# Kernel optimization log

Hardware: AMD Instinct MI355X
Metric: run time of the kernel (lower is better)

The kernel has to match this reference:

```python
import jax, jax.numpy as jnp
import numpy as np


def setup_inputs() -> dict:
    key = jax.random.key(0)
    k1, k2, k3, k4 = jax.random.split(key, 4)
    B, S, D = 4, 2048, 1024
    scale = 1.0 / np.sqrt(D)
    x = jax.random.normal(k1, (B, S, D), dtype=jnp.float32)
    Wq = jax.random.normal(k2, (D, D), dtype=jnp.float32) * scale
    Wk = jax.random.normal(k3, (D, D), dtype=jnp.float32) * scale
    Wv = jax.random.normal(k4, (D, D), dtype=jnp.float32) * scale
    return {"x": x, "Wq": Wq, "Wk": Wk, "Wv": Wv}


def reference(x, Wq, Wk, Wv):
    # x: [B, S, D]; Wq/Wk/Wv: [d_out, d_in] torch Linear convention (y = x @ W.T)
    B, S, D = x.shape
    q = jnp.einsum('bsd,od->bso', x, Wq)
    k = jnp.einsum('bsd,od->bso', x, Wk)
    v = jnp.einsum('bsd,od->bso', x, Wv)
    scores = jnp.einsum('bqo,bko->bqk', q, k)  # [B, S, S]
    causal = jnp.tril(jnp.ones((S, S), dtype=bool))  # True = keep
    scores = jnp.where(causal, scores, -jnp.inf)
    d_out = q.shape[-1]
    attn = jax.nn.softmax(scores / jnp.sqrt(jnp.asarray(d_out, x.dtype)), axis=-1)
    # dropout_prob = 0.0 -> identity
    return jnp.einsum('bqk,bko->bqo', attn, v)
```

## Files before the change

### kernel.cpp

```cpp
#include <hip/hip_runtime.h>
#include <hip/hip_bf16.h>
#include <stdint.h>

typedef __attribute__((ext_vector_type(8))) short bf16x8;
typedef __attribute__((ext_vector_type(4))) float f32x4;

__device__ __forceinline__ float bf2f(unsigned short u) {
    union { unsigned int i; float f; } z; z.i = ((unsigned int)u) << 16; return z.f;
}
__device__ __forceinline__ unsigned short f2bf(float f) {
    union { float f; unsigned int i; } z; z.f = f;
    unsigned int x = z.i;
    unsigned int r = x + 0x7fffu + ((x >> 16) & 1u);
    return (unsigned short)(r >> 16);
}

typedef const __attribute__((address_space(1))) unsigned int* gp_t;
typedef __attribute__((address_space(3))) unsigned int* lp_t;

__device__ __forceinline__ void gload_lds16(const void* g, void* l) {
    __builtin_amdgcn_global_load_lds((gp_t)g, (lp_t)l, 16, 0, 0);
}

__device__ __forceinline__ int xcd_remap(int orig, int nwg) {
    const int q = nwg >> 3, r = nwg & 7;
    const int xcd = orig & 7, pos = orig >> 3;
    return (xcd < r ? xcd * (q + 1) : r * (q + 1) + (xcd - r) * q) + pos;
}

__global__ __launch_bounds__(256) void cvt_all(
    const float* __restrict__ x, const float* __restrict__ wq,
    const float* __restrict__ wk, const float* __restrict__ wv,
    unsigned short* __restrict__ xb, unsigned short* __restrict__ wqkv) {
    const int NX = 1 << 21;
    const int DD4 = 1 << 18;
    const int total = NX + 3 * DD4;
    int i = blockIdx.x * 256 + threadIdx.x;
    const int stride = gridDim.x * 256;
    for (; i < total; i += stride) {
        const float* src;
        ushort4* dst;
        float scale = 1.0f;
        int idx;
        if (i < NX) {
            src = x; dst = (ushort4*)xb; idx = i;
        } else {
            const int j = i - NX;
            const int r = j >> 18;
            src = (r == 0) ? wq : (r == 1) ? wk : wv;
            if (r == 0) scale = 0.03125f;
            dst = (ushort4*)wqkv + (size_t)r * DD4;
            idx = j & (DD4 - 1);
            dst -= (size_t)0;
            dst += 0;
        }
        float4 v = reinterpret_cast<const float4*>(src)[idx];
        ushort4 u;
        u.x = f2bf(v.x * scale); u.y = f2bf(v.y * scale);
        u.z = f2bf(v.z * scale); u.w = f2bf(v.w * scale);
        dst[idx] = u;
    }
}

#define MFMA(a, b, c) __builtin_amdgcn_mfma_f32_16x16x32_bf16(a, b, c, 0, 0, 0)
#define SB() __builtin_amdgcn_sched_barrier(0)
#define BAR() __builtin_amdgcn_s_barrier()
#define LGKM0() asm volatile("s_waitcnt lgkmcnt(0)" ::: "memory")

__device__ __forceinline__ void gemm256_core(
    const unsigned short* __restrict__ Ab,
    const unsigned short* __restrict__ Bb,
    int m0, int n0,
    unsigned short (&As)[2][256 * 64], unsigned short (&Bs)[2][256 * 64],
    f32x4 (&acc)[8][4])
{
    constexpr int LD = 1024, NK = 16;
    const int tid = threadIdx.x;
    const int l = tid & 63, w = tid >> 6;
    const int wr = w >> 2, wc = w & 3;

    const int srow = w * 8 + (l >> 3);
    const int scol = ((l & 7) ^ (l >> 3)) * 8;
    const size_t ldst = (size_t)w * 1024 + (size_t)l * 16;

    auto stageA = [&](int t, int h, int b) {
        const unsigned short* src = Ab + (size_t)(m0 + h * 128 + srow) * LD + t * 64 + scol;
        char* dst = (char*)&As[b][0] + h * 16384 + ldst;
        gload_lds16(src, dst);
        gload_lds16(src + (size_t)64 * LD, dst + 8192);
    };
    auto stageB = [&](int t, int h, int b) {
        const unsigned short* src = Bb + (size_t)(n0 + h * 128 + srow) * LD + t * 64 + scol;
        char* dst = (char*)&Bs[b][0] + h * 16384 + ldst;
        gload_lds16(src, dst);
        gload_lds16(src + (size_t)64 * LD, dst + 8192);
    };

    const int l15 = l & 15, l7 = l & 7;
    const int s0 = (((l >> 4) ^ l7) * 16);
    const int s1 = ((((l >> 4) + 4) ^ l7) * 16);

    bf16x8 Af[4][2], Bf0[2][2], Bf1[2][2];

    stageA(0, 0, 0); stageA(0, 1, 0); stageB(0, 0, 0); stageB(0, 1, 0);
    stageB(1, 0, 1); stageB(1, 1, 1);
    asm volatile("s_waitcnt vmcnt(4)" ::: "memory");
    SB(); BAR(); SB();

    for (int t = 0; t < NK; ++t) {
        const int b = t & 1, bn = b ^ 1;
        const char* ab = (const char*)&As[b][0] + (wr * 128 + l15) * 128;
        const char* bb = (const char*)&Bs[b][0] + (wc * 64 + l15) * 128;

        #pragma unroll
        for (int mi = 0; mi < 4; ++mi) {
            Af[mi][0] = *(const bf16x8*)(ab + mi * 2048 + s0);
            Af[mi][1] = *(const bf16x8*)(ab + mi * 2048 + s1);
        }
        #pragma unroll
        for (int ni = 0; ni < 2; ++ni) {
            Bf0[ni][0] = *(const bf16x8*)(bb + ni * 2048 + s0);
            Bf0[ni][1] = *(const bf16x8*)(bb + ni * 2048 + s1);
        }
        if (t + 1 < NK) stageA(t + 1, 0, bn);
        BAR(); LGKM0(); SB();
        __builtin_amdgcn_s_setprio(1);
        #pragma unroll
        for (int mi = 0; mi < 4; ++mi)
            #pragma unroll
            for (int ni = 0; ni < 2; ++ni) {
                acc[mi][ni] = MFMA(Af[mi][0], Bf0[ni][0], acc[mi][ni]);
                acc[mi][ni] = MFMA(Af[mi][1], Bf0[ni][1], acc[mi][ni]);
            }
        __builtin_amdgcn_s_setprio(0);
        SB(); BAR(); SB();

        #pragma unroll
        for (int ni = 0; ni < 2; ++ni) {
            Bf1[ni][0] = *(const bf16x8*)(bb + 4096 + ni * 2048 + s0);
            Bf1[ni][1] = *(const bf16x8*)(bb + 4096 + ni * 2048 + s1);
        }
        if (t + 1 < NK) stageA(t + 1, 1, bn);
        BAR(); LGKM0(); SB();
        __builtin_amdgcn_s_setprio(1);
        #pragma unroll
        for (int mi = 0; mi < 4; ++mi)
            #pragma unroll
            for (int ni = 0; ni < 2; ++ni) {
                acc[mi][2 + ni] = MFMA(Af[mi][0], Bf1[ni][0], acc[mi][2 + ni]);
                acc[mi][2 + ni] = MFMA(Af[mi][1], Bf1[ni][1], acc[mi][2 + ni]);
            }
        __builtin_amdgcn_s_setprio(0);
        SB(); BAR(); SB();

        #pragma unroll
        for (int mi = 0; mi < 4; ++mi) {
            Af[mi][0] = *(const bf16x8*)(ab + 8192 + mi * 2048 + s0);
            Af[mi][1] = *(const bf16x8*)(ab + 8192 + mi * 2048 + s1);
        }
        if (t + 2 < NK) stageB(t + 2, 0, b);
        BAR(); LGKM0(); SB();
        __builtin_amdgcn_s_setprio(1);
        #pragma unroll
        for (int mi = 0; mi < 4; ++mi)
            #pragma unroll
            for (int ni = 0; ni < 2; ++ni) {
                acc[4 + mi][2 + ni] = MFMA(Af[mi][0], Bf1[ni][0], acc[4 + mi][2 + ni]);
                acc[4 + mi][2 + ni] = MFMA(Af[mi][1], Bf1[ni][1], acc[4 + mi][2 + ni]);
            }
        __builtin_amdgcn_s_setprio(0);
        SB(); BAR(); SB();

        if (t + 2 < NK) stageB(t + 2, 1, b);
        BAR(); SB();
        __builtin_amdgcn_s_setprio(1);
        #pragma unroll
        for (int mi = 0; mi < 4; ++mi)
            #pragma unroll
            for (int ni = 0; ni < 2; ++ni) {
                acc[4 + mi][ni] = MFMA(Af[mi][0], Bf0[ni][0], acc[4 + mi][ni]);
                acc[4 + mi][ni] = MFMA(Af[mi][1], Bf0[ni][1], acc[4 + mi][ni]);
            }
        __builtin_amdgcn_s_setprio(0);
        if (t + 2 < NK) {
            asm volatile("s_waitcnt vmcnt(4)" ::: "memory");
        } else if (t + 1 < NK) {
            asm volatile("s_waitcnt vmcnt(0)" ::: "memory");
        }
        SB(); BAR(); SB();
    }
}

__global__ __launch_bounds__(512, 2) void qk_proj(
    const unsigned short* __restrict__ xb, const unsigned short* __restrict__ wqkv,
    unsigned short* __restrict__ qb, unsigned short* __restrict__ kb)
{
    const int wg = xcd_remap(blockIdx.x, 256);
    const int mt = wg & 31, nt = wg >> 5;
    const int m0 = mt * 256, n0 = nt * 256;

    __shared__ unsigned short As[2][256 * 64];
    __shared__ unsigned short Bs[2][256 * 64];
    f32x4 acc[8][4] = {};

    gemm256_core(xb, wqkv, m0, n0, As, Bs, acc);

    const int tid = threadIdx.x;
    const int l = tid & 63, w = tid >> 6;
    const int wr = w >> 2, wc = w & 3;
    const int crow = (l >> 4) * 4, ccol = l & 15;
    unsigned short* C = (nt < 4) ? qb : kb;
    const int cb = (nt < 4) ? n0 : n0 - 1024;
    #pragma unroll
    for (int mi = 0; mi < 8; ++mi)
        #pragma unroll
        for (int ni = 0; ni < 4; ++ni) {
            const size_t rbase = (size_t)(m0 + wr * 128 + mi * 16 + crow);
            const size_t cg = (size_t)(cb + wc * 64 + ni * 16 + ccol);
            #pragma unroll
            for (int r = 0; r < 4; ++r)
                C[(rbase + r) * 1024 + cg] = f2bf(acc[mi][ni][r]);
        }
}

__device__ __forceinline__ void gemm128_core64(
    const unsigned short* __restrict__ Ab, int lda,
    const unsigned short* __restrict__ Bb, int ldb,
    int m0, int n0, int nk,
    unsigned short (&As)[2][128 * 64], unsigned short (&Bs)[2][128 * 64],
    f32x4 (&acc)[4][4])
{
    const int tid = threadIdx.x;
    const int l = tid & 63, w = tid >> 6;
    const int wr = w >> 1, wc = w & 1;
    const int l15 = l & 15;

    const int srow = w * 8 + (l >> 3);
    const int scol = ((l & 7) ^ (l >> 3)) * 8;
    const size_t ldst = (size_t)w * 1024 + (size_t)l * 16;

    auto stage = [&](int t, int b) {
        const int k0 = t * 64;
        #pragma unroll
        for (int i = 0; i < 4; ++i) {
            gload_lds16(Ab + (size_t)(m0 + i * 32 + srow) * lda + k0 + scol,
                        (char*)&As[b][0] + i * 4096 + ldst);
            gload_lds16(Bb + (size_t)(n0 + i * 32 + srow) * ldb + k0 + scol,
                        (char*)&Bs[b][0] + i * 4096 + ldst);
        }
    };

    const int s0 = (((l >> 4) ^ (l & 7)) * 16);
    const int s1 = ((((l >> 4) + 4) ^ (l & 7)) * 16);

    stage(0, 0);
    if (nk > 1) {
        stage(1, 1);
        asm volatile("s_waitcnt vmcnt(8)" ::: "memory");
    } else {
        asm volatile("s_waitcnt vmcnt(0)" ::: "memory");
    }
    SB(); BAR(); SB();

    for (int t = 0; t < nk; ++t) {
        const int b = t & 1;
        const char* ab = (const char*)&As[b][0] + (wr * 64 + l15) * 128;
        const char* bb = (const char*)&Bs[b][0] + (wc * 64 + l15) * 128;
        bf16x8 af[4][2], bfr[4][2];
        #pragma unroll
        for (int m = 0; m < 4; ++m) {
            af[m][0] = *(const bf16x8*)(ab + m * 2048 + s0);
            af[m][1] = *(const bf16x8*)(ab + m * 2048 + s1);
        }
        #pragma unroll
        for (int n = 0; n < 4; ++n) {
            bfr[n][0] = *(const bf16x8*)(bb + n * 2048 + s0);
            bfr[n][1] = *(const bf16x8*)(bb + n * 2048 + s1);
        }
        LGKM0(); SB();
        BAR(); SB();
        if (t + 2 < nk) stage(t + 2, b);

        __builtin_amdgcn_s_setprio(1);
        #pragma unroll
        for (int m = 0; m < 4; ++m)
            #pragma unroll
            for (int n = 0; n < 4; ++n) {
                acc[m][n] = MFMA(af[m][0], bfr[n][0], acc[m][n]);
                acc[m][n] = MFMA(af[m][1], bfr[n][1], acc[m][n]);
            }
        __builtin_amdgcn_s_setprio(0);

        if (t + 2 < nk) {
            asm volatile("s_waitcnt vmcnt(8)" ::: "memory");
        } else if (t + 1 < nk) {
            asm volatile("s_waitcnt vmcnt(0)" ::: "memory");
        }
        SB(); BAR(); SB();
    }
}

__global__ __launch_bounds__(256) void v_scores128(
    const unsigned short* __restrict__ xb, const unsigned short* __restrict__ wv,
    const unsigned short* __restrict__ qb, const unsigned short* __restrict__ kb,
    unsigned short* __restrict__ vt, unsigned short* __restrict__ sc)
{
    const int wg = xcd_remap(blockIdx.x, 1056);

    __shared__ unsigned short As[2][128 * 64];
    __shared__ unsigned short Bs[2][128 * 64];
    f32x4 acc[4][4] = {};

    const int tid = threadIdx.x;
    const int l = tid & 63, w = tid >> 6;
    const int wr = w >> 1, wc = w & 1;
    const int crow = (l >> 4) * 4, ccol = l & 15;

    if (wg < 512) {
        const int mt = wg & 63, nt = wg >> 6;
        const int m0 = mt * 128, n0 = nt * 128;
        gemm128_core64(xb, 1024, wv, 1024, m0, n0, 16, As, Bs, acc);
        #pragma unroll
        for (int m = 0; m < 4; ++m)
            #pragma unroll
            for (int n = 0; n < 4; ++n) {
                const int rbase = m0 + wr * 64 + m * 16 + crow;
                const int o = n0 + wc * 64 + n * 16 + ccol;
                ushort4 u;
                u.x = f2bf(acc[m][n][0]);
                u.y = f2bf(acc[m][n][1]);
                u.z = f2bf(acc[m][n][2]);
                u.w = f2bf(acc[m][n][3]);
                *reinterpret_cast<ushort4*>(&vt[(size_t)o * 8192 + rbase]) = u;
            }
    } else {
        const int s = wg - 512;
        const int z = s / 136, r = s % 136;
        int mt = (int)((__builtin_sqrtf(8.f * r + 1.f) - 1.f) * 0.5f);
        while ((mt + 1) * (mt + 2) / 2 <= r) ++mt;
        while (mt * (mt + 1) / 2 > r) --mt;
        const int nt = r - mt * (mt + 1) / 2;
        const int m0 = mt * 128, n0 = nt * 128;
        const unsigned short* Ab = qb + (size_t)z * 2048 * 1024;
        const unsigned short* Bb = kb + (size_t)z * 2048 * 1024;
        gemm128_core64(Ab, 1024, Bb, 1024, m0, n0, 16, As, Bs, acc);
        unsigned short* C = sc + (size_t)z * 2048 * 2048;
        #pragma unroll
        for (int m = 0; m < 4; ++m)
            #pragma unroll
            for (int n = 0; n < 4; ++n) {
                const size_t rbase = (size_t)(m0 + wr * 64 + m * 16 + crow);
                const size_t cg = (size_t)(n0 + wc * 64 + n * 16 + ccol);
                #pragma unroll
                for (int r2 = 0; r2 < 4; ++r2)
                    C[(rbase + r2) * 2048 + cg] = f2bf(acc[m][n][r2]);
            }
    }
}

__global__ __launch_bounds__(256) void gemm128_pv(
    const unsigned short* __restrict__ A, int lda, long long sA,
    const unsigned short* __restrict__ B, int ldb, long long sB,
    float* __restrict__ C, int ldc, long long sC, int K)
{
    const int orig = blockIdx.x;
    const int h = orig >> 8;
    const int c = xcd_remap(orig & 255, 256);
    const int z = c >> 6;
    const int rem = c & 63;
    const int nt = rem >> 3;
    const int j = rem & 7;
    const int mt = h ? (15 - j) : j;

    const unsigned short* Ab = A + (size_t)z * sA;
    const unsigned short* Bb = B + (size_t)z * sB;
    const int Keff = ((mt + 1) * 128 < K) ? (mt + 1) * 128 : K;
    const int nk = Keff >> 6;

    __shared__ unsigned short As[2][128 * 64];
    __shared__ unsigned short Bs[2][128 * 64];
    f32x4 acc[4][4] = {};

    gemm128_core64(Ab, lda, Bb, ldb, mt * 128, nt * 128, nk, As, Bs, acc);

    const int tid = threadIdx.x;
    const int l = tid & 63, w = tid >> 6;
    const int wr = w >> 1, wc = w & 1;
    const int crow = (l >> 4) * 4, ccol = l & 15;
    float* Cb = C + (size_t)z * sC;
    #pragma unroll
    for (int m = 0; m < 4; ++m)
        #pragma unroll
        for (int n = 0; n < 4; ++n) {
            const size_t rbase = (size_t)(mt * 128 + wr * 64 + m * 16 + crow);
            const size_t cg = (size_t)(nt * 128 + wc * 64 + n * 16 + ccol);
            #pragma unroll
            for (int r = 0; r < 4; ++r)
                Cb[(rbase + r) * ldc + cg] = acc[m][n][r];
        }
}

__global__ __launch_bounds__(256) void softmax_causal(unsigned short* __restrict__ P) {
    const int S = 2048;
    const int w = threadIdx.x >> 6, l = threadIdx.x & 63;
    const int gq = blockIdx.x * 4 + w;
    const int q = gq & (S - 1);
    unsigned short* row = P + (size_t)gq * S;
    const int wlim = ((q >> 7) + 1) << 7;
    const float NEG = -__builtin_huge_valf();

    float f[4][8];
    #pragma unroll
    for (int p = 0; p < 4; ++p) {
        const int c0 = p * 512 + l * 8;
        if (p * 512 <= q && c0 <= q) {
            uint4 rv = *reinterpret_cast<const uint4*>(row + c0);
            unsigned short us[8];
            us[0] = rv.x & 0xffff; us[1] = rv.x >> 16;
            us[2] = rv.y & 0xffff; us[3] = rv.y >> 16;
            us[4] = rv.z & 0xffff; us[5] = rv.z >> 16;
            us[6] = rv.w & 0xffff; us[7] = rv.w >> 16;
            #pragma unroll
            for (int i = 0; i < 8; ++i)
                f[p][i] = (c0 + i <= q) ? bf2f(us[i]) : NEG;
        } else {
            #pragma unroll
            for (int i = 0; i < 8; ++i) f[p][i] = NEG;
        }
    }

    float m = NEG;
    #pragma unroll
    for (int p = 0; p < 4; ++p)
        #pragma unroll
        for (int i = 0; i < 8; ++i) m = fmaxf(m, f[p][i]);
    #pragma unroll
    for (int o = 1; o < 64; o <<= 1) m = fmaxf(m, __shfl_xor(m, o));

    float s = 0.f;
    #pragma unroll
    for (int p = 0; p < 4; ++p)
        #pragma unroll
        for (int i = 0; i < 8; ++i) {
            f[p][i] = exp2f((f[p][i] - m) * 1.44269504f);
            s += f[p][i];
        }
    #pragma unroll
    for (int o = 1; o < 64; o <<= 1) s += __shfl_xor(s, o);
    const float inv = 1.0f / s;

    #pragma unroll
    for (int p = 0; p < 4; ++p) {
        const int c0 = p * 512 + l * 8;
        if (p * 512 < wlim && c0 < wlim) {
            uint4 ov;
            ov.x = f2bf(f[p][0] * inv) | ((unsigned int)f2bf(f[p][1] * inv) << 16);
            ov.y = f2bf(f[p][2] * inv) | ((unsigned int)f2bf(f[p][3] * inv) << 16);
            ov.z = f2bf(f[p][4] * inv) | ((unsigned int)f2bf(f[p][5] * inv) << 16);
            ov.w = f2bf(f[p][6] * inv) | ((unsigned int)f2bf(f[p][7] * inv) << 16);
            *reinterpret_cast<uint4*>(row + c0) = ov;
        }
    }
}

extern "C" void kernel_launch(void* const* d_in, const int* in_sizes, int n_in,
                              void* d_out, int out_size, void* d_ws, size_t ws_size,
                              hipStream_t stream) {
    const float* x  = (const float*)d_in[0];
    const float* Wq = (const float*)d_in[1];
    const float* Wk = (const float*)d_in[2];
    const float* Wv = (const float*)d_in[3];
    float* out = (float*)d_out;

    const int Bz = 4, S = 2048, D = 1024;
    const int MS = Bz * S;
    const int DD = D * D;

    char* ws = (char*)d_ws;
    unsigned short* xb   = (unsigned short*)(ws);
    unsigned short* wqkv = (unsigned short*)(ws + (16ull << 20));
    unsigned short* qb   = (unsigned short*)(ws + (22ull << 20));
    unsigned short* kb   = (unsigned short*)(ws + (38ull << 20));
    unsigned short* vt   = (unsigned short*)(ws + (54ull << 20));
    unsigned short* sc   = (unsigned short*)(ws + (70ull << 20));

    cvt_all<<<2048, 256, 0, stream>>>(x, Wq, Wk, Wv, xb, wqkv);

    qk_proj<<<256, 512, 0, stream>>>(xb, wqkv, qb, kb);

    v_scores128<<<1056, 256, 0, stream>>>(xb, wqkv + (size_t)2 * DD, qb, kb, vt, sc);

    softmax_causal<<<2048, 256, 0, stream>>>(sc);

    gemm128_pv<<<512, 256, 0, stream>>>(
        sc, S, (long long)S * S, vt, MS, S, out, D, (long long)S * D, S);
}
```

Baseline: 156.8 us.

## Fold Wq and Wk into a single weight product to skip the K projection

Uses the identity q·kᵀ = x·(Wqᵀ·Wk)·xᵀ. A small 1024x1024 GEMM first forms the combined weight Wqᵀ·Wk (with the 1/32 scale folded in), and the scores are then computed as (x·W)·xᵀ. This removes one of the two D×D projections over the 8192 tokens and drops the separate Q and K buffers. The V projection moves into the same launch as T=x·W, at the cost of a transpose kernel, an extra tiny GEMM, and an extra bf16 rounding of the product weight.

```diff
diff --git a/kernel.cpp b/kernel.cpp
--- a/kernel.cpp
+++ b/kernel.cpp
@@ -28,37 +28,61 @@
     return (xcd < r ? xcd * (q + 1) : r * (q + 1) + (xcd - r) * q) + pos;
 }
 
-__global__ __launch_bounds__(256) void cvt_all(
-    const float* __restrict__ x, const float* __restrict__ wq,
-    const float* __restrict__ wk, const float* __restrict__ wv,
-    unsigned short* __restrict__ xb, unsigned short* __restrict__ wqkv) {
+__global__ __launch_bounds__(256) void cvt_xv(const float* __restrict__ x,
+                                              const float* __restrict__ wv,
+                                              unsigned short* __restrict__ xb,
+                                              unsigned short* __restrict__ wvb) {
     const int NX = 1 << 21;
     const int DD4 = 1 << 18;
-    const int total = NX + 3 * DD4;
+    const int total = NX + DD4;
     int i = blockIdx.x * 256 + threadIdx.x;
     const int stride = gridDim.x * 256;
     for (; i < total; i += stride) {
-        const float* src;
-        ushort4* dst;
-        float scale = 1.0f;
-        int idx;
-        if (i < NX) {
-            src = x; dst = (ushort4*)xb; idx = i;
-        } else {
-            const int j = i - NX;
-            const int r = j >> 18;
-            src = (r == 0) ? wq : (r == 1) ? wk : wv;
-            if (r == 0) scale = 0.03125f;
-            dst = (ushort4*)wqkv + (size_t)r * DD4;
-            idx = j & (DD4 - 1);
-            dst -= (size_t)0;
-            dst += 0;
-        }
-        float4 v = reinterpret_cast<const float4*>(src)[idx];
+        float4 v = (i < NX) ? reinterpret_cast<const float4*>(x)[i]
+                            : reinterpret_cast<const float4*>(wv)[i - NX];
         ushort4 u;
-        u.x = f2bf(v.x * scale); u.y = f2bf(v.y * scale);
-        u.z = f2bf(v.z * scale); u.w = f2bf(v.w * scale);
-        dst[idx] = u;
+        u.x = f2bf(v.x); u.y = f2bf(v.y); u.z = f2bf(v.z); u.w = f2bf(v.w);
+        if (i < NX) reinterpret_cast<ushort4*>(xb)[i] = u;
+        else        reinterpret_cast<ushort4*>(wvb)[i - NX] = u;
+    }
+}
+
+__global__ __launch_bounds__(256) void tr_w(const float* __restrict__ wq,
+                                            const float* __restrict__ wk,
+                                            unsigned short* __restrict__ wqT,
+                                            unsigned short* __restrict__ wkT) {
+    const int id = blockIdx.x;
+    const int m = id >> 8;
+    const int t = id & 255;
+    const int tr = t >> 4, tc = t & 15;
+    const float* src = m ? wk : wq;
+    unsigned short* dst = m ? wkT : wqT;
+    const float scale = m ? 1.0f : 0.03125f;
+
+    __shared__ unsigned short tile[64][65];
+    const int tid = threadIdx.x;
+    const int r0 = tid >> 4;
+    const int c4 = tid & 15;
+    #pragma unroll
+    for (int p = 0; p < 4; ++p) {
+        const int r = p * 16 + r0;
+        float4 v = reinterpret_cast<const float4*>(
+            src + (size_t)(tr * 64 + r) * 1024 + tc * 64)[c4];
+        tile[c4 * 4 + 0][r] = f2bf(v.x * scale);
+        tile[c4 * 4 + 1][r] = f2bf(v.y * scale);
+        tile[c4 * 4 + 2][r] = f2bf(v.z * scale);
+        tile[c4 * 4 + 3][r] = f2bf(v.w * scale);
+    }
+    __syncthreads();
+    const int cr = tid >> 2;
+    const int q4 = tid & 3;
+    #pragma unroll
+    for (int p = 0; p < 4; ++p) {
+        const int off = (q4 * 4 + p) * 4;
+        ushort4 u;
+        u.x = tile[cr][off + 0]; u.y = tile[cr][off + 1];
+        u.z = tile[cr][off + 2]; u.w = tile[cr][off + 3];
+        *reinterpret_cast<ushort4*>(dst + (size_t)(tc * 64 + cr) * 1024 + tr * 64 + off) = u;
     }
 }
 
@@ -191,36 +215,55 @@
     }
 }
 
-__global__ __launch_bounds__(512, 2) void qk_proj(
-    const unsigned short* __restrict__ xb, const unsigned short* __restrict__ wqkv,
-    unsigned short* __restrict__ qb, unsigned short* __restrict__ kb)
+__global__ __launch_bounds__(512, 2) void tv_proj(
+    const unsigned short* __restrict__ xb, const unsigned short* __restrict__ wst,
+    const unsigned short* __restrict__ wvb,
+    unsigned short* __restrict__ tb, unsigned short* __restrict__ vt)
 {
     const int wg = xcd_remap(blockIdx.x, 256);
-    const int mt = wg & 31, nt = wg >> 5;
-    const int m0 = mt * 256, n0 = nt * 256;
 
     __shared__ unsigned short As[2][256 * 64];
     __shared__ unsigned short Bs[2][256 * 64];
     f32x4 acc[8][4] = {};
 
-    gemm256_core(xb, wqkv, m0, n0, As, Bs, acc);
-
     const int tid = threadIdx.x;
     const int l = tid & 63, w = tid >> 6;
     const int wr = w >> 2, wc = w & 3;
     const int crow = (l >> 4) * 4, ccol = l & 15;
-    unsigned short* C = (nt < 4) ? qb : kb;
-    const int cb = (nt < 4) ? n0 : n0 - 1024;
-    #pragma unroll
-    for (int mi = 0; mi < 8; ++mi)
-        #pragma unroll
-        for (int ni = 0; ni < 4; ++ni) {
-            const size_t rbase = (size_t)(m0 + wr * 128 + mi * 16 + crow);
-            const size_t cg = (size_t)(cb + wc * 64 + ni * 16 + ccol);
-            #pragma unroll
-            for (int r = 0; r < 4; ++r)
-                C[(rbase + r) * 1024 + cg] = f2bf(acc[mi][ni][r]);
-        }
+
+    if (wg < 128) {
+        const int mt = wg & 31, nt = wg >> 5;
+        const int m0 = mt * 256, n0 = nt * 256;
+        gemm256_core(xb, wst, m0, n0, As, Bs, acc);
+        #pragma unroll
+        for (int mi = 0; mi < 8; ++mi)
+            #pragma unroll
+            for (int ni = 0; ni < 4; ++ni) {
+                const size_t rbase = (size_t)(m0 + wr * 128 + mi * 16 + crow);
+                const size_t cg = (size_t)(n0 + wc * 64 + ni * 16 + ccol);
+                #pragma unroll
+                for (int r = 0; r < 4; ++r)
+                    tb[(rbase + r) * 1024 + cg] = f2bf(acc[mi][ni][r]);
+            }
+    } else {
+        const int v = wg - 128;
+        const int mt = v & 31, nt = v >> 5;
+        const int m0 = mt * 256, n0 = nt * 256;
+        gemm256_core(xb, wvb, m0, n0, As, Bs, acc);
+        #pragma unroll
+        for (int mi = 0; mi < 8; ++mi)
+            #pragma unroll
+            for (int ni = 0; ni < 4; ++ni) {
+                const int rbase = m0 + wr * 128 + mi * 16 + crow;
+                const int o = n0 + wc * 64 + ni * 16 + ccol;
+                ushort4 u;
+                u.x = f2bf(acc[mi][ni][0]);
+                u.y = f2bf(acc[mi][ni][1]);
+                u.z = f2bf(acc[mi][ni][2]);
+                u.w = f2bf(acc[mi][ni][3]);
+                *reinterpret_cast<ushort4*>(&vt[(size_t)o * 8192 + rbase]) = u;
+            }
+    }
 }
 
 __device__ __forceinline__ void gemm128_core64(
@@ -300,62 +343,71 @@
     }
 }
 
-__global__ __launch_bounds__(256) void v_scores128(
-    const unsigned short* __restrict__ xb, const unsigned short* __restrict__ wv,
-    const unsigned short* __restrict__ qb, const unsigned short* __restrict__ kb,
-    unsigned short* __restrict__ vt, unsigned short* __restrict__ sc)
+__global__ __launch_bounds__(256) void wst128(
+    const unsigned short* __restrict__ wkT, const unsigned short* __restrict__ wqT,
+    unsigned short* __restrict__ wst)
 {
-    const int wg = xcd_remap(blockIdx.x, 1056);
+    const int wg = xcd_remap(blockIdx.x, 64);
+    const int mt = wg & 7, nt = wg >> 3;
+    const int m0 = mt * 128, n0 = nt * 128;
 
     __shared__ unsigned short As[2][128 * 64];
     __shared__ unsigned short Bs[2][128 * 64];
     f32x4 acc[4][4] = {};
 
+    gemm128_core64(wkT, 1024, wqT, 1024, m0, n0, 16, As, Bs, acc);
+
     const int tid = threadIdx.x;
     const int l = tid & 63, w = tid >> 6;
     const int wr = w >> 1, wc = w & 1;
     const int crow = (l >> 4) * 4, ccol = l & 15;
-
-    if (wg < 512) {
-        const int mt = wg & 63, nt = wg >> 6;
-        const int m0 = mt * 128, n0 = nt * 128;
-        gemm128_core64(xb, 1024, wv, 1024, m0, n0, 16, As, Bs, acc);
-        #pragma unroll
-        for (int m = 0; m < 4; ++m)
-            #pragma unroll
-            for (int n = 0; n < 4; ++n) {
-                const int rbase = m0 + wr * 64 + m * 16 + crow;
-                const int o = n0 + wc * 64 + n * 16 + ccol;
-                ushort4 u;
-                u.x = f2bf(acc[m][n][0]);
-                u.y = f2bf(acc[m][n][1]);
-                u.z = f2bf(acc[m][n][2]);
-                u.w = f2bf(acc[m][n][3]);
-                *reinterpret_cast<ushort4*>(&vt[(size_t)o * 8192 + rbase]) = u;
-            }
-    } else {
-        const int s = wg - 512;
-        const int z = s / 136, r = s % 136;
-        int mt = (int)((__builtin_sqrtf(8.f * r + 1.f) - 1.f) * 0.5f);
-        while ((mt + 1) * (mt + 2) / 2 <= r) ++mt;
-        while (mt * (mt + 1) / 2 > r) --mt;
-        const int nt = r - mt * (mt + 1) / 2;
-        const int m0 = mt * 128, n0 = nt * 128;
-        const unsigned short* Ab = qb + (size_t)z * 2048 * 1024;
-        const unsigned short* Bb = kb + (size_t)z * 2048 * 1024;
-        gemm128_core64(Ab, 1024, Bb, 1024, m0, n0, 16, As, Bs, acc);
-        unsigned short* C = sc + (size_t)z * 2048 * 2048;
-        #pragma unroll
-        for (int m = 0; m < 4; ++m)
-            #pragma unroll
-            for (int n = 0; n < 4; ++n) {
-                const size_t rbase = (size_t)(m0 + wr * 64 + m * 16 + crow);
-                const size_t cg = (size_t)(n0 + wc * 64 + n * 16 + ccol);
-                #pragma unroll
-                for (int r2 = 0; r2 < 4; ++r2)
-                    C[(rbase + r2) * 2048 + cg] = f2bf(acc[m][n][r2]);
-            }
-    }
+    #pragma unroll
+    for (int m = 0; m < 4; ++m)
+        #pragma unroll
+        for (int n = 0; n < 4; ++n) {
+            const size_t rbase = (size_t)(m0 + wr * 64 + m * 16 + crow);
+            const size_t cg = (size_t)(n0 + wc * 64 + n * 16 + ccol);
+            #pragma unroll
+            for (int r = 0; r < 4; ++r)
+                wst[(rbase + r) * 1024 + cg] = f2bf(acc[m][n][r]);
+        }
+}
+
+__global__ __launch_bounds__(256) void scores128(
+    const unsigned short* __restrict__ tb, const unsigned short* __restrict__ xb,
+    unsigned short* __restrict__ sc)
+{
+    const int wg = xcd_remap(blockIdx.x, 544);
+
+    __shared__ unsigned short As[2][128 * 64];
+    __shared__ unsigned short Bs[2][128 * 64];
+    f32x4 acc[4][4] = {};
+
+    const int z = wg / 136, r = wg % 136;
+    int mt = (int)((__builtin_sqrtf(8.f * r + 1.f) - 1.f) * 0.5f);
+    while ((mt + 1) * (mt + 2) / 2 <= r) ++mt;
+    while (mt * (mt + 1) / 2 > r) --mt;
+    const int nt = r - mt * (mt + 1) / 2;
+    const int m0 = mt * 128, n0 = nt * 128;
+    const unsigned short* Ab = tb + (size_t)z * 2048 * 1024;
+    const unsigned short* Bb = xb + (size_t)z * 2048 * 1024;
+    gemm128_core64(Ab, 1024, Bb, 1024, m0, n0, 16, As, Bs, acc);
+
+    const int tid = threadIdx.x;
+    const int l = tid & 63, w = tid >> 6;
+    const int wr = w >> 1, wc = w & 1;
+    const int crow = (l >> 4) * 4, ccol = l & 15;
+    unsigned short* C = sc + (size_t)z * 2048 * 2048;
+    #pragma unroll
+    for (int m = 0; m < 4; ++m)
+        #pragma unroll
+        for (int n = 0; n < 4; ++n) {
+            const size_t rbase = (size_t)(m0 + wr * 64 + m * 16 + crow);
+            const size_t cg = (size_t)(n0 + wc * 64 + n * 16 + ccol);
+            #pragma unroll
+            for (int r2 = 0; r2 < 4; ++r2)
+                C[(rbase + r2) * 2048 + cg] = f2bf(acc[m][n][r2]);
+        }
 }
 
 __global__ __launch_bounds__(256) void gemm128_pv(
@@ -472,26 +524,29 @@
     const float* Wv = (const float*)d_in[3];
     float* out = (float*)d_out;
 
-    const int Bz = 4, S = 2048, D = 1024;
-    const int MS = Bz * S;
-    const int DD = D * D;
+    const int S = 2048;
 
     char* ws = (char*)d_ws;
-    unsigned short* xb   = (unsigned short*)(ws);
-    unsigned short* wqkv = (unsigned short*)(ws + (16ull << 20));
-    unsigned short* qb   = (unsigned short*)(ws + (22ull << 20));
-    unsigned short* kb   = (unsigned short*)(ws + (38ull << 20));
-    unsigned short* vt   = (unsigned short*)(ws + (54ull << 20));
-    unsigned short* sc   = (unsigned short*)(ws + (70ull << 20));
-
-    cvt_all<<<2048, 256, 0, stream>>>(x, Wq, Wk, Wv, xb, wqkv);
-
-    qk_proj<<<256, 512, 0, stream>>>(xb, wqkv, qb, kb);
-
-    v_scores128<<<1056, 256, 0, stream>>>(xb, wqkv + (size_t)2 * DD, qb, kb, vt, sc);
+    unsigned short* xb  = (unsigned short*)(ws);
+    unsigned short* wvb = (unsigned short*)(ws + (16ull << 20));
+    unsigned short* wqT = (unsigned short*)(ws + (18ull << 20));
+    unsigned short* wkT = (unsigned short*)(ws + (20ull << 20));
+    unsigned short* wst = (unsigned short*)(ws + (22ull << 20));
+    unsigned short* tb  = (unsigned short*)(ws + (24ull << 20));
+    unsigned short* vt  = (unsigned short*)(ws + (40ull << 20));
+    unsigned short* sc  = (unsigned short*)(ws + (56ull << 20));
+
+    cvt_xv<<<2048, 256, 0, stream>>>(x, Wv, xb, wvb);
+    tr_w<<<512, 256, 0, stream>>>(Wq, Wk, wqT, wkT);
+
+    wst128<<<64, 256, 0, stream>>>(wkT, wqT, wst);
+
+    tv_proj<<<256, 512, 0, stream>>>(xb, wst, wvb, tb, vt);
+
+    scores128<<<544, 256, 0, stream>>>(tb, xb, sc);
 
     softmax_causal<<<2048, 256, 0, stream>>>(sc);
 
     gemm128_pv<<<512, 256, 0, stream>>>(
-        sc, S, (long long)S * S, vt, MS, S, out, D, (long long)S * D, S);
-}
+        sc, S, (long long)S * S, vt, 8192, S, out, 1024, (long long)S * 1024, S);
+}
```

Result: faster. 144.8 us (-7.7%).
